# Performance work log

Measured on AMD Instinct MI355X. Metric: run time of the kernel, lower is better.

Reference implementation:

```python
import jax, jax.numpy as jnp
import numpy as np

T = 64      # simulation_length
B = 128     # batch
D = 2048    # flattened input dim / axons per core
N = 2048    # neurons per core
L = 4       # number of cores (chain, latency = index)
OUT = 1024  # number of output_sources


def setup_inputs() -> dict:
    key = jax.random.key(0)
    k0, k1, k2, k3 = jax.random.split(key, 4)
    x = jax.random.uniform(k0, (B, D), dtype=jnp.float32)          # rate-coded input in [0,1)
    # core_params[l] = core_matrix.transpose() -> shape [N, A]; scaled for sane membrane dynamics
    W = jax.random.normal(k1, (L, N, D), dtype=jnp.float32) * 0.05
    thresholds = jnp.ones((L,), dtype=jnp.float32)
    # axon_sources: per-core irregular gather indices into previous core's neurons (input for l=0)
    axon_idx = jax.random.randint(k2, (L, D), 0, D, dtype=jnp.int32)
    out_idx = jax.random.randint(k3, (OUT,), 0, N, dtype=jnp.int32)
    return dict(x=x, W=W, thresholds=thresholds, axon_idx=axon_idx,
                out_idx=out_idx, simulation_length=T)


def _ideal_spike_scan(avg, thr, T):
    """Per-cycle: m += avg; spike = (m > thr); m[m > thr] -= thr.  avg: [B, N]."""
    def step(m, _):
        m = m + avg
        s = (m > thr).astype(m.dtype)
        return m - thr * s, s
    _, spikes = jax.lax.scan(step, jnp.zeros_like(avg), None, length=T)
    return spikes  # [T, B, N]


def reference(x, W, thresholds, axon_idx, out_idx, simulation_length):
    T = simulation_length
    L = W.shape[0]
    # generate_input_spike_train: x replicated across all cycles -> cache[-1]
    prev = jnp.broadcast_to(x, (T,) + x.shape)  # [T, B, D]
    for l in range(L):
        # get_signal_tensor: gather axon source signals for every cycle
        gathered = prev[:, :, axon_idx[l]]                    # [T, B, A]
        # per-cycle matmul: torch.matmul(core_params, sig.T).T == sig @ W[l].T
        val = jnp.einsum('tba,na->tbn', gathered, W[l])       # [T, B, N]
        avg = val.mean(axis=0)                                # avg_values [B, N]
        # ideal membrane integrate + threshold-reset recurrence -> out spike train
        prev = _ideal_spike_scan(avg, thresholds[l], T)       # [T, B, N]
    # output_signals: sum of output-source spikes over all cycles
    return prev[:, :, out_idx].sum(axis=0)                    # [B, OUT]
```

## Files before the change

kernel.cpp:

```cpp
#include <hip/hip_runtime.h>

#define BB   128
#define DD   2048
#define NN   2048
#define LL   4
#define OUTN 1024
#define JBQ  32
#define NDIG 5
#define NSGN 4

#define NWDIG 3072
#define NG0   1024
#define NCSR  4

#define WD_NSUP 327680
#define WD_KC   10240
#define WD_J    2048

typedef double double4v __attribute__((ext_vector_type(4)));
typedef int    int4v    __attribute__((ext_vector_type(4)));
typedef char   char4v   __attribute__((ext_vector_type(4)));
typedef char   char16v  __attribute__((ext_vector_type(16)));

__device__ __forceinline__ int i8_probe_signed()
{
    const int lane = threadIdx.x & 63;
    const int hot  = ((lane >> 4) == 0) ? 1 : 0;
    int4v aFF  = {-1, -1, -1, -1};
    int4v oneh = {hot, 0, 0, 0};
    int4v d    = {0, 0, 0, 0};
    d = __builtin_amdgcn_mfma_i32_16x16x64_i8(aFF, oneh, d, 0, 0, 0);
    return d[0] < 0;
}

__global__ __launch_bounds__(256) void prep_kernel(
    const float* __restrict__ W1,
    const float* __restrict__ x,
    const int*   __restrict__ axon,
    const int*   __restrict__ oidx,
    signed char* __restrict__ Wd,
    float*       __restrict__ At,
    int*         __restrict__ off,
    int*         __restrict__ lst)
{
    __shared__ int hist[2048];
    __shared__ int part[256];

    const int t  = threadIdx.x;
    const int bk = blockIdx.x;
    const size_t DP = (size_t)NN * DD;

    if (bk < NWDIG) {
        const int l   = bk >> 10;
        const int rem = bk & 1023;
        const int nc  = rem >> 5;
        const int kc  = rem & 31;
        const int n   = nc * 64 + (t >> 2);
        const int k   = kc * 64 + (t & 3) * 16;

        const float* wp = W1 + (size_t)l * DP + (size_t)n * DD + k;
        float wv[16];
        #pragma unroll
        for (int p = 0; p < 4; ++p) {
            float4 w = *(const float4*)(wp + 4 * p);
            wv[4 * p + 0] = w.x; wv[4 * p + 1] = w.y;
            wv[4 * p + 2] = w.z; wv[4 * p + 3] = w.w;
        }
        signed char* base = Wd + (size_t)l * 5 * DP
                          + (size_t)(n >> 5) * WD_NSUP + (size_t)kc * WD_KC
                          + (n & 31) * 64 + (k & 63);

        const int sgn = i8_probe_signed();
        if (sgn) {
            int X[16];
            #pragma unroll
            for (int e = 0; e < 16; ++e) {
                int V = (int)rintf(wv[e] * 0x1p28f);
                X[e] = (int)(((unsigned)V + 0x80808080u) ^ 0x80808080u);
            }
            #pragma unroll
            for (int j = 0; j < NSGN; ++j) {
                char16v p;
                #pragma unroll
                for (int e = 0; e < 16; ++e)
                    p[e] = (char)((X[e] >> (8 * j)) & 255);
                *(char16v*)(base + (size_t)j * WD_J) = p;
            }
        } else {
            unsigned long long V[16];
            #pragma unroll
            for (int e = 0; e < 16; ++e)
                V[e] = (unsigned long long)(__double2ll_rn((double)wv[e] * 0x1p33)
                                            + (1LL << 34));
            #pragma unroll
            for (int j = 0; j < NDIG; ++j) {
                char16v p;
                #pragma unroll
                for (int e = 0; e < 16; ++e)
                    p[e] = (char)((V[e] >> (7 * j)) & 127);
                *(char16v*)(base + (size_t)j * WD_J) = p;
            }
        }
        return;
    }
    if (bk < NWDIG + NG0) {
        int i = (bk - NWDIG) * 256 + t;
        int b = i >> 11;
        int k = i & (DD - 1);
        At[(size_t)(k >> 6) * 8192 + b * 64 + (k & 63)] = x[b * DD + axon[k]];
        return;
    }
    {
        const int m   = bk - (NWDIG + NG0);
        const int* ip = (m < 3) ? (axon + (size_t)(m + 1) * DD) : oidx;
        const int cnt = (m < 3) ? DD : OUTN;
        int* offG = off + m * 2052;
        int* lstG = lst + m * 2048;

        for (int i = t; i < 2048; i += 256) hist[i] = 0;
        __syncthreads();
        for (int e = t; e < cnt; e += 256) atomicAdd(&hist[ip[e]], 1);
        __syncthreads();

        const int b0 = t * 8;
        int s = 0;
        #pragma unroll
        for (int i = 0; i < 8; ++i) s += hist[b0 + i];
        part[t] = s;
        __syncthreads();
        for (int d = 1; d < 256; d <<= 1) {
            int v = (t >= d) ? part[t - d] : 0;
            __syncthreads();
            part[t] += v;
            __syncthreads();
        }
        int base = part[t] - s;
        #pragma unroll
        for (int i = 0; i < 8; ++i) {
            int h = hist[b0 + i];
            offG[b0 + i] = base;
            hist[b0 + i] = base;
            base += h;
        }
        if (t == 255) offG[2048] = base;
        __syncthreads();
        for (int e = t; e < cnt; e += 256) {
            int n = ip[e];
            int pos = atomicAdd(&hist[n], 1);
            lstG[pos] = e;
        }
    }
}

__global__ __launch_bounds__(256, 4) void layer0_kernel(
    const float* __restrict__ Atile,
    const float* __restrict__ Wl,
    const float* __restrict__ thr,
    const int*   __restrict__ Tptr,
    const int* __restrict__ goff, const int* __restrict__ glst,
    signed char* __restrict__ g8n)
{
    __shared__ double red[4 * 64 * 4];

    const int t    = threadIdx.x;
    const int wq   = t >> 6;
    const int lane = t & 63;
    const int q    = lane >> 4;
    const int c    = lane & 15;

    const int g     = blockIdx.x;
    const int btile = (g >> 3) & 7;
    const int nsup  = (g & 7) | ((g >> 6) << 3);
    const int n0    = nsup * 16;
    const int bcol  = btile * 16 + c;

    double4v pr = {0., 0., 0., 0.}, pcv = {0., 0., 0., 0.};
    pr  = __builtin_amdgcn_mfma_f64_16x16x4f64(0.25 * (double)c, 1.0, pr, 0, 0, 0);
    pcv = __builtin_amdgcn_mfma_f64_16x16x4f64(0.25, (double)c, pcv, 0, 0, 0);
    int rowD[4], colD[4];
    #pragma unroll
    for (int r = 0; r < 4; ++r) {
        rowD[r] = (int)(pr[r] + 0.25);
        colD[r] = (int)(pcv[r] + 0.25);
    }

    double4v acc[4] = {{0.,0.,0.,0.},{0.,0.,0.,0.},{0.,0.,0.,0.},{0.,0.,0.,0.}};

    const int    kbase = wq * (DD / 4);
    const float* wb0   = Wl + (size_t)(n0 + c) * DD + kbase + 4 * q;

    float4 wv0[4], sv[4];
    #pragma unroll
    for (int p = 0; p < 4; ++p) wv0[p] = *(const float4*)(wb0 + 16 * p);
    #pragma unroll
    for (int p = 0; p < 4; ++p) {
        int kabs = kbase + 16 * p + 4 * q;
        sv[p] = *(const float4*)(Atile + (size_t)(kabs >> 6) * 8192
                                 + bcol * 64 + (kabs & 63));
    }

    for (int u = 0; u < JBQ / 4; ++u) {
        #pragma unroll
        for (int gg = 0; gg < 4; ++gg) {
            float4 w0 = wv0[gg];
            float4 s  = sv[gg];

            int jn = 4 * u + 4 + gg; if (jn > JBQ - 1) jn = JBQ - 1;
            wv0[gg] = *(const float4*)(wb0 + 16 * jn);
            int kabs = kbase + 16 * jn + 4 * q;
            sv[gg] = *(const float4*)(Atile + (size_t)(kabs >> 6) * 8192
                                      + bcol * 64 + (kabs & 63));

            acc[0] = __builtin_amdgcn_mfma_f64_16x16x4f64((double)w0.x, (double)s.x, acc[0], 0, 0, 0);
            acc[1] = __builtin_amdgcn_mfma_f64_16x16x4f64((double)w0.y, (double)s.y, acc[1], 0, 0, 0);
            acc[2] = __builtin_amdgcn_mfma_f64_16x16x4f64((double)w0.z, (double)s.z, acc[2], 0, 0, 0);
            acc[3] = __builtin_amdgcn_mfma_f64_16x16x4f64((double)w0.w, (double)s.w, acc[3], 0, 0, 0);
        }
    }

    double4v a0 = (acc[0] + acc[1]) + (acc[2] + acc[3]);
    {
        double* my = red + ((size_t)wq * 64 + lane) * 4;
        #pragma unroll
        for (int r = 0; r < 4; ++r) my[r] = a0[r];
    }
    __syncthreads();
    if (wq == 0) {
        double a[4];
        #pragma unroll
        for (int r = 0; r < 4; ++r) {
            a[r] =  red[((size_t)0 * 64 + lane) * 4 + r];
            a[r] += red[((size_t)1 * 64 + lane) * 4 + r];
            a[r] += red[((size_t)2 * 64 + lane) * 4 + r];
            a[r] += red[((size_t)3 * 64 + lane) * 4 + r];
        }

        const double th = (double)thr[0];
        const int T = *Tptr;
        double m0 = 0., m1 = 0., m2 = 0., m3 = 0.;
        int c0 = 0, c1 = 0, c2 = 0, c3 = 0;
        for (int tt = 0; tt < T; ++tt) {
            m0 += a[0]; if (m0 > th) { c0++; m0 -= th; }
            m1 += a[1]; if (m1 > th) { c1++; m1 -= th; }
            m2 += a[2]; if (m2 > th) { c2++; m2 -= th; }
            m3 += a[3]; if (m3 > th) { c3++; m3 -= th; }
        }
        int cnt[4] = {c0, c1, c2, c3};
        #pragma unroll
        for (int r = 0; r < 4; ++r) {
            int n = n0 + rowD[r];
            int b = btile * 16 + colD[r];
            for (int j = goff[n]; j < goff[n + 1]; ++j) {
                int k = glst[j];
                g8n[(size_t)(k >> 6) * 8192 + b * 64 + (k & 63)] =
                    (signed char)cnt[r];
            }
        }
    }
}

__global__ __launch_bounds__(256, 4) void layer_i8_kernel(
    const signed char* __restrict__ B8,
    const signed char* __restrict__ Wd5,
    const float* __restrict__ thr, int l,
    const int*   __restrict__ Tptr,
    const int* __restrict__ goff, const int* __restrict__ glst,
    signed char* __restrict__ g8n,
    const int* __restrict__ ooff, const int* __restrict__ olst,
    float* __restrict__ outp)
{
    __shared__ double red[4 * 64 * 4];

    const int t    = threadIdx.x;
    const int wq   = t >> 6;
    const int lane = t & 63;
    const int q    = lane >> 4;
    const int c    = lane & 15;

    const int g     = blockIdx.x;
    const int btile = (g >> 3) & 7;
    const int nsup  = (g & 7) | ((g >> 6) << 3);
    const int n0    = nsup * 16;
    const int bcol  = btile * 16 + c;

    const int sgn = i8_probe_signed();

    int rowD[4], colD[4];
    {
        const int cb  = c * 0x01010101;
        const int hot = (q == 0) ? 1 : 0;
        int4v aLab = {cb, cb, cb, cb};
        int4v oneh = {hot, 0, 0, 0};
        int4v dR = {0, 0, 0, 0}, dC = {0, 0, 0, 0};
        dR = __builtin_amdgcn_mfma_i32_16x16x64_i8(aLab, oneh, dR, 0, 0, 0);
        dC = __builtin_amdgcn_mfma_i32_16x16x64_i8(oneh, aLab, dC, 0, 0, 0);
        #pragma unroll
        for (int r = 0; r < 4; ++r) { rowD[r] = dR[r]; colD[r] = dC[r]; }
    }

    int4v acc[NDIG], accS = (int4v)0;
    #pragma unroll
    for (int j = 0; j < NDIG; ++j) acc[j] = (int4v)0;

    const signed char* ab = Wd5 + (size_t)(nsup >> 1) * WD_NSUP
                          + (nsup & 1) * 1024 + c * 64 + q * 16;
    const signed char* bb = B8 + bcol * 64 + q * 16;

    const int4v ones = {0x01010101, 0x01010101, 0x01010101, 0x01010101};
    const int ck0 = wq * 8;

    if (sgn) {
        #pragma unroll 1
        for (int kc = 0; kc < 8; ++kc) {
            const signed char* ap = ab + (size_t)(ck0 + kc) * WD_KC;
            int4v A[NSGN], Bv;
            #pragma unroll
            for (int j = 0; j < NSGN; ++j)
                A[j] = *(const int4v*)(ap + (size_t)j * WD_J);
            Bv = *(const int4v*)(bb + (size_t)(ck0 + kc) * 8192);
            #pragma unroll
            for (int j = 0; j < NSGN; ++j)
                acc[j] = __builtin_amdgcn_mfma_i32_16x16x64_i8(A[j], Bv, acc[j], 0, 0, 0);
        }
        const double T0 = 0x1p-28, T1 = 0x1p-20, T2 = 0x1p-12, T3 = 0x1p-4;
        double* my = red + ((size_t)wq * 64 + lane) * 4;
        #pragma unroll
        for (int r = 0; r < 4; ++r)
            my[r] = T0 * (double)acc[0][r] + T1 * (double)acc[1][r]
                  + T2 * (double)acc[2][r] + T3 * (double)acc[3][r];
    } else {
        #pragma unroll 1
        for (int kc = 0; kc < 8; ++kc) {
            const signed char* ap = ab + (size_t)(ck0 + kc) * WD_KC;
            int4v A[NDIG], Bv;
            #pragma unroll
            for (int j = 0; j < NDIG; ++j)
                A[j] = *(const int4v*)(ap + (size_t)j * WD_J);
            Bv = *(const int4v*)(bb + (size_t)(ck0 + kc) * 8192);
            #pragma unroll
            for (int j = 0; j < NDIG; ++j)
                acc[j] = __builtin_amdgcn_mfma_i32_16x16x64_i8(A[j], Bv, acc[j], 0, 0, 0);
            accS = __builtin_amdgcn_mfma_i32_16x16x64_i8(ones, Bv, accS, 0, 0, 0);
        }
        const double S0 = 0x1p-33, S1 = 0x1p-26, S2 = 0x1p-19,
                     S3 = 0x1p-12, S4 = 0x1p-5;
        double* my = red + ((size_t)wq * 64 + lane) * 4;
        #pragma unroll
        for (int r = 0; r < 4; ++r)
            my[r] = S0 * (double)acc[0][r] + S1 * (double)acc[1][r]
                  + S2 * (double)acc[2][r] + S3 * (double)acc[3][r]
                  + S4 * (double)acc[4][r] - 2.0 * (double)accS[r];
    }
    __syncthreads();
    if (wq == 0) {
        double a[4];
        #pragma unroll
        for (int r = 0; r < 4; ++r) {
            a[r] =  red[((size_t)0 * 64 + lane) * 4 + r];
            a[r] += red[((size_t)1 * 64 + lane) * 4 + r];
            a[r] += red[((size_t)2 * 64 + lane) * 4 + r];
            a[r] += red[((size_t)3 * 64 + lane) * 4 + r];
        }

        const double th = (double)thr[l];
        const int T = *Tptr;
        const double invT = 1.0 / (double)T;
        double m0 = 0., m1 = 0., m2 = 0., m3 = 0.;
        int c0 = 0, c1 = 0, c2 = 0, c3 = 0;
        const double v0 = a[0] * invT, v1 = a[1] * invT,
                     v2 = a[2] * invT, v3 = a[3] * invT;
        for (int tt = 0; tt < T; ++tt) {
            m0 += v0; if (m0 > th) { c0++; m0 -= th; }
            m1 += v1; if (m1 > th) { c1++; m1 -= th; }
            m2 += v2; if (m2 > th) { c2++; m2 -= th; }
            m3 += v3; if (m3 > th) { c3++; m3 -= th; }
        }
        int cnt[4] = {c0, c1, c2, c3};
        #pragma unroll
        for (int r = 0; r < 4; ++r) {
            int n = n0 + rowD[r];
            int b = btile * 16 + colD[r];
            if (goff) {
                for (int j = goff[n]; j < goff[n + 1]; ++j) {
                    int k = glst[j];
                    g8n[(size_t)(k >> 6) * 8192 + b * 64 + (k & 63)] =
                        (signed char)cnt[r];
                }
            }
            if (ooff) {
                for (int j = ooff[n]; j < ooff[n + 1]; ++j)
                    outp[(size_t)b * OUTN + olst[j]] = (float)cnt[r];
            }
        }
    }
}

__global__ __launch_bounds__(256, 2) void layer_kernel(
    const float* __restrict__ src,
    const int*   __restrict__ idx,
    int sR, int sB,
    const float* __restrict__ Wl,
    const float* __restrict__ thresholds, int l,
    const int*   __restrict__ Tptr,
    float* __restrict__ dst, int isLast)
{
    __shared__ double red[4 * 64 * 8];

    const int t    = threadIdx.x;
    const int wq   = t >> 6;
    const int lane = t & 63;
    const int q    = lane >> 4;
    const int c    = lane & 15;

    const int g     = blockIdx.x;
    const int btile = (g >> 3) & 7;
    const int nsup  = (g & 7) | ((g >> 6) << 3);
    const int n0    = nsup * 32;
    const int bcol  = btile * 16 + c;
    const size_t bo = (size_t)bcol * sB;

    double4v pr = {0., 0., 0., 0.}, pcv = {0., 0., 0., 0.};
    pr  = __builtin_amdgcn_mfma_f64_16x16x4f64(0.25 * (double)c, 1.0, pr, 0, 0, 0);
    pcv = __builtin_amdgcn_mfma_f64_16x16x4f64(0.25, (double)c, pcv, 0, 0, 0);
    int rowD[4], colD[4];
    #pragma unroll
    for (int r = 0; r < 4; ++r) {
        rowD[r] = (int)(pr[r] + 0.25);
        colD[r] = (int)(pcv[r] + 0.25);
    }

    double4v acc0[4] = {{0.,0.,0.,0.},{0.,0.,0.,0.},{0.,0.,0.,0.},{0.,0.,0.,0.}};
    double4v acc1[4] = {{0.,0.,0.,0.},{0.,0.,0.,0.},{0.,0.,0.,0.},{0.,0.,0.,0.}};

    const int    kbase = wq * (DD / 4);
    const float* wb0   = Wl + (size_t)(n0 + c) * DD + kbase + 4 * q;
    const float* wb1   = wb0 + (size_t)16 * DD;
    const int*   ibase = idx ? (idx + kbase + 4 * q) : nullptr;

    float4 wv0[4], wv1[4];
    float4 sv[4];
    int4   iv[4];

    #pragma unroll
    for (int p = 0; p < 4; ++p) {
        wv0[p] = *(const float4*)(wb0 + 16 * p);
        wv1[p] = *(const float4*)(wb1 + 16 * p);
    }
    #pragma unroll
    for (int p = 0; p < 4; ++p) {
        int r0, r1, r2, r3;
        if (ibase) {
            int4 iv0 = *(const int4*)(ibase + 16 * p);
            r0 = iv0.x; r1 = iv0.y; r2 = iv0.z; r3 = iv0.w;
        } else {
            int kb = kbase + 16 * p + 4 * q;
            r0 = kb; r1 = kb + 1; r2 = kb + 2; r3 = kb + 3;
        }
        sv[p].x = src[(size_t)r0 * sR + bo];
        sv[p].y = src[(size_t)r1 * sR + bo];
        sv[p].z = src[(size_t)r2 * sR + bo];
        sv[p].w = src[(size_t)r3 * sR + bo];
    }
    if (ibase) {
        #pragma unroll
        for (int p = 0; p < 4; ++p) iv[p] = *(const int4*)(ibase + 16 * (4 + p));
    }

    for (int u = 0; u < JBQ / 4; ++u) {
        #pragma unroll
        for (int gg = 0; gg < 4; ++gg) {
            float4 w0 = wv0[gg];
            float4 w1 = wv1[gg];
            float4 s  = sv[gg];

            int jn = 4 * u + 4 + gg; if (jn > JBQ - 1) jn = JBQ - 1;
            wv0[gg] = *(const float4*)(wb0 + 16 * jn);
            wv1[gg] = *(const float4*)(wb1 + 16 * jn);

            int r0, r1, r2, r3;
            if (ibase) {
                int4 ivv = iv[gg];
                r0 = ivv.x; r1 = ivv.y; r2 = ivv.z; r3 = ivv.w;
            } else {
                int kb = kbase + 16 * jn + 4 * q;
                r0 = kb; r1 = kb + 1; r2 = kb + 2; r3 = kb + 3;
            }
            sv[gg].x = src[(size_t)r0 * sR + bo];
            sv[gg].y = src[(size_t)r1 * sR + bo];
            sv[gg].z = src[(size_t)r2 * sR + bo];
            sv[gg].w = src[(size_t)r3 * sR + bo];

            if (ibase) {
                int jm = 4 * u + 8 + gg; if (jm > JBQ - 1) jm = JBQ - 1;
                iv[gg] = *(const int4*)(ibase + 16 * jm);
            }

            acc0[0] = __builtin_amdgcn_mfma_f64_16x16x4f64((double)w0.x, (double)s.x, acc0[0], 0, 0, 0);
            acc1[0] = __builtin_amdgcn_mfma_f64_16x16x4f64((double)w1.x, (double)s.x, acc1[0], 0, 0, 0);
            acc0[1] = __builtin_amdgcn_mfma_f64_16x16x4f64((double)w0.y, (double)s.y, acc0[1], 0, 0, 0);
            acc1[1] = __builtin_amdgcn_mfma_f64_16x16x4f64((double)w1.y, (double)s.y, acc1[1], 0, 0, 0);
            acc0[2] = __builtin_amdgcn_mfma_f64_16x16x4f64((double)w0.z, (double)s.z, acc0[2], 0, 0, 0);
            acc1[2] = __builtin_amdgcn_mfma_f64_16x16x4f64((double)w1.z, (double)s.z, acc1[2], 0, 0, 0);
            acc0[3] = __builtin_amdgcn_mfma_f64_16x16x4f64((double)w0.w, (double)s.w, acc0[3], 0, 0, 0);
            acc1[3] = __builtin_amdgcn_mfma_f64_16x16x4f64((double)w1.w, (double)s.w, acc1[3], 0, 0, 0);
        }
    }

    double4v a0 = (acc0[0] + acc0[1]) + (acc0[2] + acc0[3]);
    double4v a1 = (acc1[0] + acc1[1]) + (acc1[2] + acc1[3]);

    {
        double* my = red + ((size_t)wq * 64 + lane) * 8;
        #pragma unroll
        for (int r = 0; r < 4; ++r) { my[r] = a0[r]; my[4 + r] = a1[r]; }
    }
    __syncthreads();
    if (wq < 2) {
        const int off = wq * 4;
        double a[4];
        #pragma unroll
        for (int r = 0; r < 4; ++r) {
            a[r] =  red[((size_t)0 * 64 + lane) * 8 + off + r];
            a[r] += red[((size_t)1 * 64 + lane) * 8 + off + r];
            a[r] += red[((size_t)2 * 64 + lane) * 8 + off + r];
            a[r] += red[((size_t)3 * 64 + lane) * 8 + off + r];
        }

        const double th = (double)thresholds[l];
        const int T = *Tptr;
        const float sc = isLast ? 1.0f : (1.0f / (float)T);
        double m0 = 0., m1 = 0., m2 = 0., m3 = 0.;
        int c0 = 0, c1 = 0, c2 = 0, c3 = 0;
        for (int tt = 0; tt < T; ++tt) {
            m0 += a[0]; if (m0 > th) { c0++; m0 -= th; }
            m1 += a[1]; if (m1 > th) { c1++; m1 -= th; }
            m2 += a[2]; if (m2 > th) { c2++; m2 -= th; }
            m3 += a[3]; if (m3 > th) { c3++; m3 -= th; }
        }
        int cnt[4] = {c0, c1, c2, c3};
        #pragma unroll
        for (int r = 0; r < 4; ++r) {
            int n = n0 + 16 * wq + rowD[r];
            int b = btile * 16 + colD[r];
            dst[(size_t)n * BB + b] = (float)cnt[r] * sc;
        }
    }
}

__global__ __launch_bounds__(256) void out_kernel(
    const float* __restrict__ cntT, const int* __restrict__ out_idx,
    float* __restrict__ out)
{
    int i = blockIdx.x * 256 + threadIdx.x;
    int b = i >> 10;
    int o = i & 1023;
    out[i] = cntT[(size_t)out_idx[o] * BB + b];
}

extern "C" void kernel_launch(void* const* d_in, const int* in_sizes, int n_in,
                              void* d_out, int out_size, void* d_ws, size_t ws_size,
                              hipStream_t stream)
{
    const float* x    = (const float*)d_in[0];
    const float* W    = (const float*)d_in[1];
    const float* thr  = (const float*)d_in[2];
    const int*   axon = (const int*)d_in[3];
    const int*   oidx = (const int*)d_in[4];
    const int*   Tptr = (const int*)d_in[5];
    float* out = (float*)d_out;

    const size_t DP = (size_t)NN * DD;
    char* ws = (char*)d_ws;
    float* At   = (float*)ws;
    float* mA   = (float*)(ws + (1u << 20));
    float* mB   = (float*)(ws + (2u << 20));
    float* cntT = (float*)(ws + (3u << 20));
    signed char* g8A = (signed char*)(ws + (4u << 20));
    signed char* g8B = (signed char*)(ws + (4u << 20) + (256u << 10));
    int* off = (int*)(ws + (4u << 20) + (512u << 10));
    int* lst = (int*)(ws + (4u << 20) + (640u << 10));
    signed char* Wd  = (signed char*)(ws + (5u << 20));

    const int useI8 = (ws_size >= ((size_t)80 << 20)) ? 1 : 0;

    if (!useI8) {
        const float* srcs[LL] = { x, mA, mB, mA };
        float*       dsts[LL] = { mA, mB, mA, cntT };
        for (int l = 0; l < LL; ++l) {
            layer_kernel<<<512, 256, 0, stream>>>(
                srcs[l], axon + (size_t)l * DD,
                (l == 0) ? 1 : BB, (l == 0) ? DD : 1,
                W + (size_t)l * NN * DD, thr, l, Tptr,
                dsts[l], (l == LL - 1) ? 1 : 0);
        }
        out_kernel<<<(BB * OUTN) / 256, 256, 0, stream>>>(cntT, oidx, out);
        return;
    }

    prep_kernel<<<NWDIG + NG0 + NCSR, 256, 0, stream>>>(
        W + DP, x, axon, oidx, Wd, At, off, lst);

    layer0_kernel<<<1024, 256, 0, stream>>>(
        At, W, thr, Tptr, off + 0 * 2052, lst + 0 * 2048, g8A);

    layer_i8_kernel<<<1024, 256, 0, stream>>>(
        g8A, Wd + 0 * 5 * DP, thr, 1, Tptr,
        off + 1 * 2052, lst + 1 * 2048, g8B,
        nullptr, nullptr, nullptr);
    layer_i8_kernel<<<1024, 256, 0, stream>>>(
        g8B, Wd + 1 * 5 * DP, thr, 2, Tptr,
        off + 2 * 2052, lst + 2 * 2048, g8A,
        nullptr, nullptr, nullptr);
    layer_i8_kernel<<<1024, 256, 0, stream>>>(
        g8A, Wd + 2 * 5 * DP, thr, 3, Tptr,
        nullptr, nullptr, nullptr,
        off + 3 * 2052, lst + 3 * 2048, out);
}
```

Before: 207.3 us.

## Move layer 0 to int8 MFMA with digit-split weights and three-plane input

Layer 0 previously ran an FP64 MFMA GEMM on float weights and a gathered float input tile. It now also uses int8 digit-decomposed weights: the prep kernel converts all four layers' weights and quantizes the gathered input to 22-bit fixed point split into three byte planes. Layer 0 accumulates 4x3 int8 MFMA partial products and recombines them in double with power-of-two scales. The goal is to replace the slow FP64 MFMA path with high-throughput int8 MFMA, at the cost of a larger prep kernel, more workspace, and quantization of the input, which could flip spike threshold decisions.

```diff
diff --git a/kernel.cpp b/kernel.cpp
--- a/kernel.cpp
+++ b/kernel.cpp
@@ -5,17 +5,18 @@
 #define NN   2048
 #define LL   4
 #define OUTN 1024
-#define JBQ  32
 #define NDIG 5
 #define NSGN 4
-
-#define NWDIG 3072
+#define NXP  3
+
+#define NWDIG 4096
 #define NG0   1024
 #define NCSR  4
 
 #define WD_NSUP 327680
 #define WD_KC   10240
 #define WD_J    2048
+#define XPLANE  262144
 
 typedef double double4v __attribute__((ext_vector_type(4)));
 typedef int    int4v    __attribute__((ext_vector_type(4)));
@@ -34,12 +35,12 @@
 }
 
 __global__ __launch_bounds__(256) void prep_kernel(
-    const float* __restrict__ W1,
+    const float* __restrict__ W,
     const float* __restrict__ x,
     const int*   __restrict__ axon,
     const int*   __restrict__ oidx,
     signed char* __restrict__ Wd,
-    float*       __restrict__ At,
+    signed char* __restrict__ xd,
     int*         __restrict__ off,
     int*         __restrict__ lst)
 {
@@ -58,7 +59,7 @@
         const int n   = nc * 64 + (t >> 2);
         const int k   = kc * 64 + (t & 3) * 16;
 
-        const float* wp = W1 + (size_t)l * DP + (size_t)n * DD + k;
+        const float* wp = W + (size_t)l * DP + (size_t)n * DD + k;
         float wv[16];
         #pragma unroll
         for (int p = 0; p < 4; ++p) {
@@ -107,7 +108,12 @@
         int i = (bk - NWDIG) * 256 + t;
         int b = i >> 11;
         int k = i & (DD - 1);
-        At[(size_t)(k >> 6) * 8192 + b * 64 + (k & 63)] = x[b * DD + axon[k]];
+        int V = (int)rintf(x[b * DD + axon[k]] * 0x1p22f);
+        unsigned X = ((unsigned)V + 0x808080u) ^ 0x808080u;
+        size_t pos = (size_t)(k >> 6) * 8192 + b * 64 + (k & 63);
+        xd[pos]              = (signed char)(X & 255);
+        xd[XPLANE + pos]     = (signed char)((X >> 8) & 255);
+        xd[2 * XPLANE + pos] = (signed char)((X >> 16) & 255);
         return;
     }
     {
@@ -152,9 +158,9 @@
     }
 }
 
-__global__ __launch_bounds__(256, 4) void layer0_kernel(
-    const float* __restrict__ Atile,
-    const float* __restrict__ Wl,
+__global__ __launch_bounds__(256, 4) void layer0_i8_kernel(
+    const signed char* __restrict__ xd,
+    const signed char* __restrict__ Wd0,
     const float* __restrict__ thr,
     const int*   __restrict__ Tptr,
     const int* __restrict__ goff, const int* __restrict__ glst,
@@ -174,55 +180,61 @@
     const int n0    = nsup * 16;
     const int bcol  = btile * 16 + c;
 
-    double4v pr = {0., 0., 0., 0.}, pcv = {0., 0., 0., 0.};
-    pr  = __builtin_amdgcn_mfma_f64_16x16x4f64(0.25 * (double)c, 1.0, pr, 0, 0, 0);
-    pcv = __builtin_amdgcn_mfma_f64_16x16x4f64(0.25, (double)c, pcv, 0, 0, 0);
     int rowD[4], colD[4];
+    {
+        const int cb  = c * 0x01010101;
+        const int hot = (q == 0) ? 1 : 0;
+        int4v aLab = {cb, cb, cb, cb};
+        int4v oneh = {hot, 0, 0, 0};
+        int4v dR = {0, 0, 0, 0}, dC = {0, 0, 0, 0};
+        dR = __builtin_amdgcn_mfma_i32_16x16x64_i8(aLab, oneh, dR, 0, 0, 0);
+        dC = __builtin_amdgcn_mfma_i32_16x16x64_i8(oneh, aLab, dC, 0, 0, 0);
+        #pragma unroll
+        for (int r = 0; r < 4; ++r) { rowD[r] = dR[r]; colD[r] = dC[r]; }
+    }
+
+    int4v acc[NSGN * NXP];
     #pragma unroll
-    for (int r = 0; r < 4; ++r) {
-        rowD[r] = (int)(pr[r] + 0.25);
-        colD[r] = (int)(pcv[r] + 0.25);
-    }
-
-    double4v acc[4] = {{0.,0.,0.,0.},{0.,0.,0.,0.},{0.,0.,0.,0.},{0.,0.,0.,0.}};
-
-    const int    kbase = wq * (DD / 4);
-    const float* wb0   = Wl + (size_t)(n0 + c) * DD + kbase + 4 * q;
-
-    float4 wv0[4], sv[4];
-    #pragma unroll
-    for (int p = 0; p < 4; ++p) wv0[p] = *(const float4*)(wb0 + 16 * p);
-    #pragma unroll
-    for (int p = 0; p < 4; ++p) {
-        int kabs = kbase + 16 * p + 4 * q;
-        sv[p] = *(const float4*)(Atile + (size_t)(kabs >> 6) * 8192
-                                 + bcol * 64 + (kabs & 63));
-    }
-
-    for (int u = 0; u < JBQ / 4; ++u) {
-        #pragma unroll
-        for (int gg = 0; gg < 4; ++gg) {
-            float4 w0 = wv0[gg];
-            float4 s  = sv[gg];
-
-            int jn = 4 * u + 4 + gg; if (jn > JBQ - 1) jn = JBQ - 1;
-            wv0[gg] = *(const float4*)(wb0 + 16 * jn);
-            int kabs = kbase + 16 * jn + 4 * q;
-            sv[gg] = *(const float4*)(Atile + (size_t)(kabs >> 6) * 8192
-                                      + bcol * 64 + (kabs & 63));
-
-            acc[0] = __builtin_amdgcn_mfma_f64_16x16x4f64((double)w0.x, (double)s.x, acc[0], 0, 0, 0);
-            acc[1] = __builtin_amdgcn_mfma_f64_16x16x4f64((double)w0.y, (double)s.y, acc[1], 0, 0, 0);
-            acc[2] = __builtin_amdgcn_mfma_f64_16x16x4f64((double)w0.z, (double)s.z, acc[2], 0, 0, 0);
-            acc[3] = __builtin_amdgcn_mfma_f64_16x16x4f64((double)w0.w, (double)s.w, acc[3], 0, 0, 0);
-        }
-    }
-
-    double4v a0 = (acc[0] + acc[1]) + (acc[2] + acc[3]);
+    for (int j = 0; j < NSGN * NXP; ++j) acc[j] = (int4v)0;
+
+    const signed char* ab = Wd0 + (size_t)(nsup >> 1) * WD_NSUP
+                          + (nsup & 1) * 1024 + c * 64 + q * 16;
+    const signed char* xb = xd + bcol * 64 + q * 16;
+
+    const int ck0 = wq * 8;
+
+    #pragma unroll 1
+    for (int kc = 0; kc < 8; ++kc) {
+        const signed char* ap = ab + (size_t)(ck0 + kc) * WD_KC;
+        const signed char* bp = xb + (size_t)(ck0 + kc) * 8192;
+        int4v A[NSGN], Bv[NXP];
+        #pragma unroll
+        for (int i = 0; i < NSGN; ++i)
+            A[i] = *(const int4v*)(ap + (size_t)i * WD_J);
+        #pragma unroll
+        for (int j = 0; j < NXP; ++j)
+            Bv[j] = *(const int4v*)(bp + (size_t)j * XPLANE);
+        #pragma unroll
+        for (int i = 0; i < NSGN; ++i)
+            #pragma unroll
+            for (int j = 0; j < NXP; ++j)
+                acc[i * NXP + j] = __builtin_amdgcn_mfma_i32_16x16x64_i8(
+                    A[i], Bv[j], acc[i * NXP + j], 0, 0, 0);
+    }
+
+    const double Wt[6] = {0x1p-50, 0x1p-42, 0x1p-34, 0x1p-26, 0x1p-18, 0x1p-10};
     {
         double* my = red + ((size_t)wq * 64 + lane) * 4;
         #pragma unroll
-        for (int r = 0; r < 4; ++r) my[r] = a0[r];
+        for (int r = 0; r < 4; ++r) {
+            double s = 0.;
+            #pragma unroll
+            for (int i = 0; i < NSGN; ++i)
+                #pragma unroll
+                for (int j = 0; j < NXP; ++j)
+                    s += Wt[i + j] * (double)acc[i * NXP + j][r];
+            my[r] = s;
+        }
     }
     __syncthreads();
     if (wq == 0) {
@@ -466,14 +478,14 @@
         for (int p = 0; p < 4; ++p) iv[p] = *(const int4*)(ibase + 16 * (4 + p));
     }
 
-    for (int u = 0; u < JBQ / 4; ++u) {
+    for (int u = 0; u < 8; ++u) {
         #pragma unroll
         for (int gg = 0; gg < 4; ++gg) {
             float4 w0 = wv0[gg];
             float4 w1 = wv1[gg];
             float4 s  = sv[gg];
 
-            int jn = 4 * u + 4 + gg; if (jn > JBQ - 1) jn = JBQ - 1;
+            int jn = 4 * u + 4 + gg; if (jn > 31) jn = 31;
             wv0[gg] = *(const float4*)(wb0 + 16 * jn);
             wv1[gg] = *(const float4*)(wb1 + 16 * jn);
 
@@ -491,7 +503,7 @@
             sv[gg].w = src[(size_t)r3 * sR + bo];
 
             if (ibase) {
-                int jm = 4 * u + 8 + gg; if (jm > JBQ - 1) jm = JBQ - 1;
+                int jm = 4 * u + 8 + gg; if (jm > 31) jm = 31;
                 iv[gg] = *(const int4*)(ibase + 16 * jm);
             }
 
@@ -571,7 +583,7 @@
 
     const size_t DP = (size_t)NN * DD;
     char* ws = (char*)d_ws;
-    float* At   = (float*)ws;
+    signed char* xd = (signed char*)ws;
     float* mA   = (float*)(ws + (1u << 20));
     float* mB   = (float*)(ws + (2u << 20));
     float* cntT = (float*)(ws + (3u << 20));
@@ -581,7 +593,7 @@
     int* lst = (int*)(ws + (4u << 20) + (640u << 10));
     signed char* Wd  = (signed char*)(ws + (5u << 20));
 
-    const int useI8 = (ws_size >= ((size_t)80 << 20)) ? 1 : 0;
+    const int useI8 = (ws_size >= ((size_t)96 << 20)) ? 1 : 0;
 
     if (!useI8) {
         const float* srcs[LL] = { x, mA, mB, mA };
@@ -598,21 +610,22 @@
     }
 
     prep_kernel<<<NWDIG + NG0 + NCSR, 256, 0, stream>>>(
-        W + DP, x, axon, oidx, Wd, At, off, lst);
-
-    layer0_kernel<<<1024, 256, 0, stream>>>(
-        At, W, thr, Tptr, off + 0 * 2052, lst + 0 * 2048, g8A);
+        W, x, axon, oidx, Wd, xd, off, lst);
+
+    layer0_i8_kernel<<<1024, 256, 0, stream>>>(
+        xd, Wd + 0 * 5 * DP, thr, Tptr,
+        off + 0 * 2052, lst + 0 * 2048, g8A);
 
     layer_i8_kernel<<<1024, 256, 0, stream>>>(
-        g8A, Wd + 0 * 5 * DP, thr, 1, Tptr,
+        g8A, Wd + 1 * 5 * DP, thr, 1, Tptr,
         off + 1 * 2052, lst + 1 * 2048, g8B,
         nullptr, nullptr, nullptr);
     layer_i8_kernel<<<1024, 256, 0, stream>>>(
-        g8B, Wd + 1 * 5 * DP, thr, 2, Tptr,
+        g8B, Wd + 2 * 5 * DP, thr, 2, Tptr,
         off + 2 * 2052, lst + 2 * 2048, g8A,
         nullptr, nullptr, nullptr);
     layer_i8_kernel<<<1024, 256, 0, stream>>>(
-        g8A, Wd + 2 * 5 * DP, thr, 3, Tptr,
+        g8A, Wd + 3 * 5 * DP, thr, 3, Tptr,
         nullptr, nullptr, nullptr,
         off + 3 * 2052, lst + 3 * 2048, out);
 }
```

Result: faster. 198.7 us (-4.1%).
